# Kernel tuning notes

Hardware: AMD Instinct MI355X
Metric: run time of the kernel (lower is better)

The kernel has to match this reference:

```python
import jax, jax.numpy as jnp
import numpy as np
from jax import lax

ROUTING_ITERS = 3
EPS = 1e-8


def _conv(x, w, b, stride=1):
    # x: [B,C,H,W], w: [O,C,kh,kw]  (VALID padding, NCHW/OIHW)
    y = lax.conv_general_dilated(x, w, (stride, stride), 'VALID',
                                 dimension_numbers=('NCHW', 'OIHW', 'NCHW'))
    return y + b[None, :, None, None]


def _maxpool2(x):
    return lax.reduce_window(x, -jnp.inf, lax.max, (1, 1, 2, 2), (1, 1, 2, 2), 'VALID')


def _squash(s, axis=-1):
    n2 = jnp.sum(s * s, axis=axis, keepdims=True)
    return s * (n2 / (1.0 + n2)) / jnp.sqrt(n2 + EPS)


def setup_inputs() -> dict:
    key = jax.random.key(0)
    ks = jax.random.split(key, 9)
    p = lambda k, shp: (jax.random.normal(k, shp, dtype=jnp.float32) * 0.05)
    return {
        'x':  jax.random.normal(ks[0], (64, 1, 92, 92), dtype=jnp.float32),
        'w1': p(ks[1], (128, 1, 9, 9)),   'b1': jnp.zeros((128,), jnp.float32),
        'w2': p(ks[2], (64, 128, 5, 5)),  'b2': jnp.zeros((64,), jnp.float32),
        'wc': p(ks[3], (128, 64, 8, 8)),  'bc': jnp.zeros((128,), jnp.float32),
        # routing transform: [num_primary=1024, num_sar=10, out_dim=16, in_dim=32]
        'Wr': p(ks[4], (1024, 10, 16, 32)),
    }


def reference(x, w1, b1, w2, b2, wc, bc, Wr):
    B = x.shape[0]
    # feature extractor (dropout is identity at inference)
    h = jax.nn.relu(_conv(x, w1, b1))          # [B,128,84,84]
    h = _maxpool2(h)                            # [B,128,42,42]
    h = _conv(h, w2, b2)                        # [B,64,38,38]
    # primary capsule conv
    h = _conv(h, wc, bc, stride=2)              # [B,128,16,16]
    # 128 channels = 4 capsule types * 32-dim capsules, 16x16 spatial -> 1024 caps
    u = h.reshape(B, 4, 32, 16, 16).transpose(0, 1, 3, 4, 2).reshape(B, 1024, 32)
    u = _squash(u)                              # [B,1024,32]
    # u_hat: predictions of each primary cap for each SAR cap
    u_hat = jnp.einsum('bpi,ptoi->bpto', u, Wr)  # [B,1024,10,16]
    # dynamic routing
    b_log = jnp.zeros((B, 1024, 10), dtype=x.dtype)
    for _ in range(ROUTING_ITERS):
        c = jax.nn.softmax(b_log, axis=2)               # [B,1024,10]
        s = jnp.einsum('bpt,bpto->bto', c, u_hat)       # [B,10,16]
        v = _squash(s)                                   # [B,10,16]
        b_log = b_log + jnp.einsum('bpto,bto->bpt', u_hat, v)
    likelihood = jnp.sqrt(jnp.sum(v * v, axis=-1) + EPS)  # [B,10]
    return likelihood
```

## Files before the change

kernel.cpp:

```cpp
#include <hip/hip_runtime.h>
#include <hip/hip_bf16.h>
#include <math.h>


#define EPSF 1e-8f

typedef __bf16 bf16x8 __attribute__((ext_vector_type(8)));
typedef __bf16 bf16x4 __attribute__((ext_vector_type(4)));
typedef float floatx4 __attribute__((ext_vector_type(4)));
typedef float floatx16 __attribute__((ext_vector_type(16)));

__global__ __launch_bounds__(256) void k_t_all(const float* __restrict__ Wr,
                                               const float* __restrict__ wc,
                                               const float* __restrict__ w2,
                                               const float* __restrict__ w1,
                                               __bf16* __restrict__ wrb,
                                               __bf16* __restrict__ wca,
                                               __bf16* __restrict__ w2a,
                                               __bf16* __restrict__ w1b) {
    int i = blockIdx.x * 256 + threadIdx.x;
    if (i < 5242880) {
        wrb[i] = (__bf16)Wr[i];
        return;
    }
    int i2 = i - 5242880;
    if (i2 < 524288) {
        int j = i2 & 7, lane = (i2 >> 3) & 63, f = i2 >> 9;
        int ct = f & 3, ks = (f >> 2) & 1, khw = (f >> 3) & 63, icc = f >> 9;
        int c32 = lane & 31, h = lane >> 5;
        int oc = ct * 32 + c32;
        int ic = icc * 32 + ks * 16 + h * 8 + j;
        wca[i2] = (__bf16)wc[(oc * 64 + ic) * 64 + khw];
        return;
    }
    int i3 = i2 - 524288;
    if (i3 < 204800) {
        int j = i3 & 7, lane = (i3 >> 3) & 63, f = i3 >> 9;
        int mt = f & 1, ks = (f >> 1) & 3, rem = f >> 3;
        int khw = rem % 25, icc = rem / 25;
        int c32 = lane & 31, h = lane >> 5;
        int oc = mt * 32 + c32;
        int ic = icc * 64 + ks * 16 + h * 8 + j;
        w2a[i3] = (__bf16)w2[(oc * 128 + ic) * 25 + khw];
        return;
    }
    int i4 = i3 - 204800;
    if (i4 < 12288) {
        int kt = i4 >> 10, oc = (i4 >> 3) & 127, j = i4 & 7;
        int k = kt * 8 + j;
        w1b[i4] = (__bf16)(k < 81 ? w1[oc * 81 + k] : 0.f);
    }
}

__global__ __launch_bounds__(256, 3) void k_conv1_mfma(const float* __restrict__ x,
                                                       const __bf16* __restrict__ w1b,
                                                       const float* __restrict__ b1,
                                                       __bf16* __restrict__ h1n) {
    __shared__ float xs[960];
    __shared__ __bf16 Bl[18432];
    int py = blockIdx.x, b = blockIdx.y;
    int t = threadIdx.x;
    int lane = t & 63, w = t >> 6;
    int cc = lane & 15, q = lane >> 4;

    const float* xb = x + (size_t)b * 8464 + 2 * py * 92;
    for (int j = t; j < 920; j += 256) xs[j] = xb[j];

    bf16x8 af2[2][3];
#pragma unroll
    for (int g2 = 0; g2 < 2; ++g2)
#pragma unroll
        for (int ks = 0; ks < 3; ++ks)
            af2[g2][ks] = *(const bf16x8*)(w1b + ((ks * 4 + q) * 128 + g2 * 64 + w * 16 + cc) * 8);

    __syncthreads();

    if (t < 192) {
        int row = t / 96, pos = t - (t / 96) * 96;
        int sbase = row * 92 + pos;
        bool pvalid = pos < 84;
#pragma unroll
        for (int kt = 0; kt < 12; ++kt) {
            bf16x8 pk;
#pragma unroll
            for (int j = 0; j < 8; ++j) {
                int k = kt * 8 + j;
                int kh = k / 9, kw = k - kh * 9;
                float v = (pvalid && k < 81) ? xs[sbase + kh * 92 + kw] : 0.f;
                pk[j] = (__bf16)v;
            }
            *(bf16x8*)(Bl + ((kt * 2 + row) * 96 + pos) * 8) = pk;
        }
    }
    __syncthreads();

    floatx4 acc[2][2][6];
#pragma unroll
    for (int g2 = 0; g2 < 2; ++g2)
#pragma unroll
        for (int rr = 0; rr < 2; ++rr)
#pragma unroll
            for (int n6 = 0; n6 < 6; ++n6)
                acc[g2][rr][n6] = (floatx4){0.f, 0.f, 0.f, 0.f};

    const char* Bb = (const char*)Bl + cc * 16 + q * 3072;
#pragma unroll
    for (int rr = 0; rr < 2; ++rr)
#pragma unroll
        for (int n6 = 0; n6 < 6; ++n6) {
#pragma unroll
            for (int ks = 0; ks < 3; ++ks) {
                bf16x8 bf = *(const bf16x8*)(Bb + ks * 12288 + rr * 1536 + n6 * 256);
                acc[0][rr][n6] = __builtin_amdgcn_mfma_f32_16x16x32_bf16(af2[0][ks], bf, acc[0][rr][n6], 0, 0, 0);
                acc[1][rr][n6] = __builtin_amdgcn_mfma_f32_16x16x32_bf16(af2[1][ks], bf, acc[1][rr][n6], 0, 0, 0);
            }
        }

#pragma unroll
    for (int g2 = 0; g2 < 2; ++g2) {
        int oc0 = g2 * 64 + w * 16 + q * 4;
        float4 bv = *(const float4*)(b1 + oc0);
        size_t obase = (((size_t)b * 42 + py) * 42) * 128 + oc0;
#pragma unroll
        for (int n6 = 0; n6 < 6; ++n6) {
            bf16x4 pk;
#pragma unroll
            for (int r = 0; r < 4; ++r) {
                float vert = fmaxf(acc[g2][0][n6][r], acc[g2][1][n6][r]);
                float hz = fmaxf(vert, __shfl_xor(vert, 1, 64));
                float pooled = fmaxf(hz + ((const float*)&bv)[r], 0.f);
                pk[r] = (__bf16)pooled;
            }
            if ((cc & 1) == 0) {
                int px = n6 * 8 + (cc >> 1);
                if (px < 42)
                    *(bf16x4*)(h1n + obase + (size_t)px * 128) = pk;
            }
        }
    }
}

__global__ __launch_bounds__(256) void k_conv2(const __bf16* __restrict__ h1n,
                                               const __bf16* __restrict__ w2a,
                                               float* __restrict__ p01) {
    __shared__ __bf16 ins[25704];
    int g = blockIdx.x, b = blockIdx.y, icc = blockIdx.z;
    int row0 = g * 5;
    int t = threadIdx.x;
    int lane = t & 63, w = t >> 6;
    int c32 = lane & 31, h = lane >> 5;
    int validp = (g < 7) ? 190 : 114;
    int ic0 = icc * 64;

    int baseN[2], posi[2];
#pragma unroll
    for (int nt = 0; nt < 2; ++nt) {
        int pi = (w * 2 + nt) * 32 + c32;
        int pc = pi < validp ? pi : validp - 1;
        int r = pc / 38, c = pc - r * 38;
        posi[nt] = pi;
        baseN[nt] = (r * 42 + c) * 136 + h * 16;
    }

#pragma unroll
    for (int half = 0; half < 2; ++half) {
        uint4 rb[6];
        int lo[6];
#pragma unroll
        for (int k = 0; k < 6; ++k) {
            int j = (half * 6 + k) * 256 + t;
            if (j > 3023) j -= 256;
            int lr = j / 336, rem = j - lr * 336;
            int ix = rem >> 3, sb = rem & 7;
            int rg = row0 + lr; if (rg > 41) rg = 41;
            rb[k] = *(const uint4*)(h1n + ((((size_t)b * 42 + rg) * 42 + ix) * 128 + ic0 + sb * 8));
            lo[k] = (lr * 42 + ix) * 136 + sb * 16;
        }
#pragma unroll
        for (int k = 0; k < 6; ++k)
            *(uint4*)((char*)ins + lo[k]) = rb[k];
    }

    floatx16 acc[2][2];
#pragma unroll
    for (int mt = 0; mt < 2; ++mt)
#pragma unroll
        for (int nt = 0; nt < 2; ++nt)
#pragma unroll
            for (int i = 0; i < 16; ++i) acc[mt][nt][i] = 0.f;

    const __bf16* wic = w2a + (size_t)icc * 25 * 4096 + (lane << 3);

    bf16x8 abuf[3][8];
#pragma unroll
    for (int ks = 0; ks < 4; ++ks) {
        abuf[0][ks * 2]     = *(const bf16x8*)(wic + 0 * 4096 + ks * 1024);
        abuf[0][ks * 2 + 1] = *(const bf16x8*)(wic + 0 * 4096 + ks * 1024 + 512);
        abuf[1][ks * 2]     = *(const bf16x8*)(wic + 1 * 4096 + ks * 1024);
        abuf[1][ks * 2 + 1] = *(const bf16x8*)(wic + 1 * 4096 + ks * 1024 + 512);
    }

    __syncthreads();
#pragma unroll
    for (int khw = 0; khw < 25; ++khw) {
        if (khw + 2 < 25) {
            const __bf16* wk2 = wic + (khw + 2) * 4096;
#pragma unroll
            for (int ks = 0; ks < 4; ++ks) {
                abuf[(khw + 2) % 3][ks * 2]     = *(const bf16x8*)(wk2 + ks * 1024);
                abuf[(khw + 2) % 3][ks * 2 + 1] = *(const bf16x8*)(wk2 + ks * 1024 + 512);
            }
        }
        int kh = khw / 5, kw = khw - kh * 5;
        int doff = (kh * 42 + kw) * 136;
#pragma unroll
        for (int ks = 0; ks < 4; ++ks) {
            bf16x8 a0 = abuf[khw % 3][ks * 2];
            bf16x8 a1 = abuf[khw % 3][ks * 2 + 1];
#pragma unroll
            for (int nt = 0; nt < 2; ++nt) {
                bf16x8 bfr = *(const bf16x8*)((char*)ins + baseN[nt] + doff + ks * 32);
                acc[0][nt] = __builtin_amdgcn_mfma_f32_32x32x16_bf16(a0, bfr, acc[0][nt], 0, 0, 0);
                acc[1][nt] = __builtin_amdgcn_mfma_f32_32x32x16_bf16(a1, bfr, acc[1][nt], 0, 0, 0);
            }
        }
    }
    float* pdst = p01 + (size_t)icc * 5914624;
#pragma unroll
    for (int nt = 0; nt < 2; ++nt) {
        int pi = posi[nt];
        if (pi < validp) {
            int r = pi / 38, c = pi - r * 38;
            int oh = row0 + r;
            size_t obase = (((size_t)b * 38 + oh) * 38 + c) * 64;
#pragma unroll
            for (int mt = 0; mt < 2; ++mt) {
#pragma unroll
                for (int g2 = 0; g2 < 4; ++g2) {
                    int oc0 = mt * 32 + g2 * 8 + h * 4;
                    floatx4 pv;
                    pv[0] = acc[mt][nt][g2 * 4 + 0];
                    pv[1] = acc[mt][nt][g2 * 4 + 1];
                    pv[2] = acc[mt][nt][g2 * 4 + 2];
                    pv[3] = acc[mt][nt][g2 * 4 + 3];
                    *(floatx4*)(pdst + obase + oc0) = pv;
                }
            }
        }
    }
}

__global__ __launch_bounds__(256) void k_reduce_h2(const float* __restrict__ p01,
                                                   const float* __restrict__ b2,
                                                   __bf16* __restrict__ h2n) {
    int i = blockIdx.x * 256 + threadIdx.x;
    if (i >= 1478656) return;
    size_t e = (size_t)i * 4;
    floatx4 a = *(const floatx4*)(p01 + e);
    floatx4 b = *(const floatx4*)(p01 + 5914624 + e);
    floatx4 bv = *(const floatx4*)(b2 + ((i * 4) & 63));
    bf16x4 pk;
    pk.x = (__bf16)(a[0] + b[0] + bv[0]);
    pk.y = (__bf16)(a[1] + b[1] + bv[1]);
    pk.z = (__bf16)(a[2] + b[2] + bv[2]);
    pk.w = (__bf16)(a[3] + b[3] + bv[3]);
    *(bf16x4*)(h2n + e) = pk;
}

__global__ __launch_bounds__(256, 4) void k_convcaps(const __bf16* __restrict__ h2n,
                                                     const __bf16* __restrict__ wca,
                                                     float* __restrict__ pc) {
    __shared__ __bf16 ins[13680];
    int g = blockIdx.x, b = blockIdx.y, icc = blockIdx.z;
    int t = threadIdx.x;
    int lane = t & 63, ct = t >> 6;
    int c32 = lane & 31, h = lane >> 5;
    int rloc = c32 >> 4, cx = c32 & 15;
    int ic0 = icc * 32;

    floatx16 acc;
#pragma unroll
    for (int i = 0; i < 16; ++i) acc[i] = 0.f;

    int Bbase = (76 * rloc + cx) * 72 + h * 16;
    {
        uint4 rb[6];
        int lo[6];
#pragma unroll
        for (int k = 0; k < 6; ++k) {
            int j = k * 256 + t;
            if (j > 1519) j -= 256;
            int r = j / 152, rem = j - r * 152;
            int c = rem >> 2, s = rem & 3;
            rb[k] = *(const uint4*)(h2n + ((((size_t)b * 38 + 4 * g + r) * 38 + c) * 64 + ic0 + s * 8));
            int X = (r * 2 + (c & 1)) * 19 + (c >> 1);
            lo[k] = X * 72 + s * 16;
        }
#pragma unroll
        for (int k = 0; k < 6; ++k)
            *(uint4*)((char*)ins + lo[k]) = rb[k];
    }
    __syncthreads();
    const __bf16* wic = wca + ((size_t)icc * 64 * 8 + ct) * 512 + (lane << 3);
#pragma unroll
    for (int khw = 0; khw < 64; ++khw) {
        int kh = khw >> 3, kw = khw & 7;
        int par = kw & 1, k2 = kw >> 1;
        int doff = ((kh * 2 + par) * 19 + k2) * 72;
        const __bf16* wk = wic + khw * 4096;
#pragma unroll
        for (int ks = 0; ks < 2; ++ks) {
            bf16x8 af = *(const bf16x8*)(wk + ks * 2048);
            bf16x8 bfr = *(const bf16x8*)((char*)ins + Bbase + doff + ks * 32);
            acc = __builtin_amdgcn_mfma_f32_32x32x16_bf16(af, bfr, acc, 0, 0, 0);
        }
    }
    int pos = (2 * g + rloc) * 16 + cx;
    float* dst = pc + (size_t)icc * 2097152 + (((size_t)b * 1024 + ct * 256 + pos) * 32);
#pragma unroll
    for (int g2 = 0; g2 < 4; ++g2) {
        floatx4 pv;
        pv[0] = acc[g2 * 4 + 0];
        pv[1] = acc[g2 * 4 + 1];
        pv[2] = acc[g2 * 4 + 2];
        pv[3] = acc[g2 * 4 + 3];
        *(floatx4*)(dst + g2 * 8 + h * 4) = pv;
    }
}

__global__ __launch_bounds__(256) void k_squash(const float* __restrict__ pc,
                                                const float* __restrict__ bc,
                                                __bf16* __restrict__ ub) {
    int i = blockIdx.x * 256 + threadIdx.x;
    if (i >= 65536) return;
    int ct = (i >> 8) & 3;
    const float* p0 = pc + (size_t)i * 32;
    const float* p1 = pc + 2097152 + (size_t)i * 32;
    const float* bv = bc + ct * 32;
    float vals[32];
    float n2 = 0.f;
#pragma unroll
    for (int k = 0; k < 8; ++k) {
        floatx4 a = *(const floatx4*)(p0 + k * 4);
        floatx4 b = *(const floatx4*)(p1 + k * 4);
        floatx4 bb = *(const floatx4*)(bv + k * 4);
#pragma unroll
        for (int e = 0; e < 4; ++e) {
            float v = a[e] + b[e] + bb[e];
            vals[k * 4 + e] = v;
            n2 = fmaf(v, v, n2);
        }
    }
    float scale = (n2 / (1.f + n2)) / sqrtf(n2 + EPSF);
    __bf16* dst = ub + (size_t)i * 32;
#pragma unroll
    for (int k = 0; k < 8; ++k) {
        bf16x4 pk;
        pk.x = (__bf16)(vals[k * 4 + 0] * scale);
        pk.y = (__bf16)(vals[k * 4 + 1] * scale);
        pk.z = (__bf16)(vals[k * 4 + 2] * scale);
        pk.w = (__bf16)(vals[k * 4 + 3] * scale);
        *(bf16x4*)(dst + k * 4) = pk;
    }
}

__global__ __launch_bounds__(256, 2) void k_uhat(const __bf16* __restrict__ ub,
                                                 const __bf16* __restrict__ wrb,
                                                 __bf16* __restrict__ uhT) {
    int pt = blockIdx.x, ts = blockIdx.y, bz = blockIdx.z;
    int t = threadIdx.x;
    int p = pt * 64 + (t & 63);
    int q = t >> 6;
    bf16x8 wf[4][4];
#pragma unroll
    for (int o4 = 0; o4 < 4; ++o4)
#pragma unroll
        for (int j = 0; j < 4; ++j)
            wf[o4][j] = *(const bf16x8*)(wrb + (((size_t)p * 10 + ts) * 16 + q * 4 + o4) * 32 + j * 8);
#pragma unroll 1
    for (int bi = 0; bi < 16; ++bi) {
        int b = bz * 16 + bi;
        bf16x8 uf[4];
        const bf16x8* up = (const bf16x8*)(ub + ((size_t)b * 1024 + p) * 32);
#pragma unroll
        for (int j = 0; j < 4; ++j) uf[j] = up[j];
        float sv[4];
#pragma unroll
        for (int o4 = 0; o4 < 4; ++o4) {
            float s = 0.f;
#pragma unroll
            for (int j = 0; j < 4; ++j)
#pragma unroll
                for (int e = 0; e < 8; ++e)
                    s = fmaf((float)uf[j][e], (float)wf[o4][j][e], s);
            sv[o4] = s;
        }
        bf16x4 pk;
        pk.x = (__bf16)sv[0];
        pk.y = (__bf16)sv[1];
        pk.z = (__bf16)sv[2];
        pk.w = (__bf16)sv[3];
        *(bf16x4*)(uhT + ((((size_t)b * 10 + ts) * 1024 + p) * 16 + q * 4)) = pk;
    }
}

#define UHS_ADDR(P, HF) ((((P) << 5) + ((HF) << 4)) ^ ((((P) >> 2) & 7) << 4))
__global__ __launch_bounds__(256) void k_route(const __bf16* __restrict__ uhT,
                                               const float* __restrict__ blR,
                                               float* __restrict__ blW,
                                               float* __restrict__ out,
                                               int first, int dob, int last) {
    __shared__ __bf16 uh_s[16384];
    __shared__ float sred[4][16];
    __shared__ float vs[16];
    int b = blockIdx.x, tt = blockIdx.y;
    int t = threadIdx.x;
    const __bf16* uhb = uhT + ((size_t)b * 10 + tt) * 16384;
#pragma unroll
    for (int k = 0; k < 8; ++k) {
        int j = k * 256 + t;
        *(uint4*)((char*)uh_s + UHS_ADDR(j >> 1, j & 1)) =
            *(const uint4*)((const char*)uhb + j * 16);
    }
    __syncthreads();

    float acc[16];
#pragma unroll
    for (int o = 0; o < 16; ++o) acc[o] = 0.f;
    const float* blb = blR + b * 10240;
    for (int p = t; p < 1024; p += 256) {
        float c;
        if (first) {
            c = 0.1f;
        } else {
            float den = 0.f, et = 0.f;
#pragma unroll
            for (int tp = 0; tp < 10; ++tp) {
                float e = expf(blb[tp * 1024 + p]);
                den += e;
                if (tp == tt) et = e;
            }
            c = et / den;
        }
        bf16x8 u0 = *(const bf16x8*)((char*)uh_s + UHS_ADDR(p, 0));
        bf16x8 u1 = *(const bf16x8*)((char*)uh_s + UHS_ADDR(p, 1));
#pragma unroll
        for (int o = 0; o < 8; ++o) {
            acc[o]     = fmaf(c, (float)u0[o], acc[o]);
            acc[8 + o] = fmaf(c, (float)u1[o], acc[8 + o]);
        }
    }
    int lane = t & 63, wid = t >> 6;
#pragma unroll
    for (int o = 0; o < 16; ++o) {
        float v = acc[o];
#pragma unroll
        for (int off = 32; off >= 1; off >>= 1) v += __shfl_xor(v, off, 64);
        if (lane == 0) sred[wid][o] = v;
    }
    __syncthreads();
    if (t < 16) {
        float s = (sred[0][t] + sred[1][t]) + (sred[2][t] + sred[3][t]);
        float n2 = s * s;
#pragma unroll
        for (int off = 1; off < 16; off <<= 1) n2 += __shfl_xor(n2, off, 16);
        float scale = (n2 / (1.f + n2)) / sqrtf(n2 + EPSF);
        vs[t] = s * scale;
        if (last && t == 0) {
            float sv2 = n2 * scale * scale;
            out[b * 10 + tt] = sqrtf(sv2 + EPSF);
        }
    }
    __syncthreads();

    if (dob) {
        const float* blr = blR + (b * 10 + tt) * 1024;
        float* blw = blW + (b * 10 + tt) * 1024;
        for (int p = t; p < 1024; p += 256) {
            bf16x8 u0 = *(const bf16x8*)((char*)uh_s + UHS_ADDR(p, 0));
            bf16x8 u1 = *(const bf16x8*)((char*)uh_s + UHS_ADDR(p, 1));
            float d = 0.f;
#pragma unroll
            for (int o = 0; o < 8; ++o) {
                d = fmaf((float)u0[o], vs[o], d);
                d = fmaf((float)u1[o], vs[8 + o], d);
            }
            blw[p] = first ? d : (blr[p] + d);
        }
    }
}

extern "C" void kernel_launch(void* const* d_in, const int* in_sizes, int n_in,
                              void* d_out, int out_size, void* d_ws, size_t ws_size,
                              hipStream_t stream) {
    const float* x  = (const float*)d_in[0];
    const float* w1 = (const float*)d_in[1];
    const float* b1 = (const float*)d_in[2];
    const float* w2 = (const float*)d_in[3];
    const float* b2 = (const float*)d_in[4];
    const float* wc = (const float*)d_in[5];
    const float* bc = (const float*)d_in[6];
    const float* Wr = (const float*)d_in[7];
    float* out = (float*)d_out;
    float* ws  = (float*)d_ws;

    __bf16* w2a = (__bf16*)(ws);
    __bf16* wca = (__bf16*)(ws + 102400);
    __bf16* w1b = (__bf16*)(ws + 364544);
    __bf16* h1n = (__bf16*)(ws + 375040);
    __bf16* h2n = (__bf16*)(ws + 7600384);
    __bf16* ub  = (__bf16*)(ws + 12654848);
    float*  blA = ws + 14752000;
    __bf16* wrb = (__bf16*)(ws + 15417600);
    float*  p01 = ws + 18039040;
    float*  pc  = ws + 18039040;
    float*  blB = ws + 29868288;
    __bf16* uhT = (__bf16*)(ws + 375040);

    k_t_all<<<23376, 256, 0, stream>>>(Wr, wc, w2, w1, wrb, wca, w2a, w1b);
    k_conv1_mfma<<<dim3(42, 64), 256, 0, stream>>>(x, w1b, b1, h1n);
    k_conv2<<<dim3(8, 64, 2), 256, 0, stream>>>(h1n, w2a, p01);
    k_reduce_h2<<<5776, 256, 0, stream>>>(p01, b2, h2n);
    k_convcaps<<<dim3(8, 64, 2), 256, 0, stream>>>(h2n, wca, pc);
    k_squash<<<256, 256, 0, stream>>>(pc, bc, ub);
    k_uhat<<<dim3(16, 10, 4), 256, 0, stream>>>(ub, wrb, uhT);
    k_route<<<dim3(64, 10), 256, 0, stream>>>(uhT, blA, blA, out, 1, 1, 0);
    k_route<<<dim3(64, 10), 256, 0, stream>>>(uhT, blA, blB, out, 0, 1, 0);
    k_route<<<dim3(64, 10), 256, 0, stream>>>(uhT, blB, blB, out, 0, 0, 1);
}
```

Measured before the change: 283.0 us.

## Compute u_hat with bf16 MFMA using pre-swizzled routing weights

Replaces the scalar FMA u_hat kernel with one that issues a 16x16x32 bf16 MFMA per (primary capsule, SAR type). The weight-conversion kernel now writes Wr in an MFMA fragment layout so each lane loads one contiguous 8-element vector. Each wave handles 16 batch columns, and the grid becomes 64x10 blocks without a batch split. This trades the register-resident weight reuse across batches for matrix-core throughput and a changed memory access pattern.

```diff
diff --git a/kernel.cpp b/kernel.cpp
--- a/kernel.cpp
+++ b/kernel.cpp
@@ -20,7 +20,10 @@
                                                __bf16* __restrict__ w1b) {
     int i = blockIdx.x * 256 + threadIdx.x;
     if (i < 5242880) {
-        wrb[i] = (__bf16)Wr[i];
+        int e = i & 7, l = (i >> 3) & 63;
+        int pt_ = i >> 9;
+        int o = l & 15, k = (l >> 4) * 8 + e;
+        wrb[i] = (__bf16)Wr[((size_t)pt_ * 16 + o) * 32 + k];
         return;
     }
     int i2 = i - 5242880;
@@ -364,43 +367,29 @@
     }
 }
 
-__global__ __launch_bounds__(256, 2) void k_uhat(const __bf16* __restrict__ ub,
-                                                 const __bf16* __restrict__ wrb,
-                                                 __bf16* __restrict__ uhT) {
-    int pt = blockIdx.x, ts = blockIdx.y, bz = blockIdx.z;
+__global__ __launch_bounds__(256) void k_uhat(const __bf16* __restrict__ ub,
+                                              const __bf16* __restrict__ wrf,
+                                              __bf16* __restrict__ uhT) {
+    int pg = blockIdx.x, ts = blockIdx.y;
     int t = threadIdx.x;
-    int p = pt * 64 + (t & 63);
-    int q = t >> 6;
-    bf16x8 wf[4][4];
-#pragma unroll
-    for (int o4 = 0; o4 < 4; ++o4)
-#pragma unroll
-        for (int j = 0; j < 4; ++j)
-            wf[o4][j] = *(const bf16x8*)(wrb + (((size_t)p * 10 + ts) * 16 + q * 4 + o4) * 32 + j * 8);
-#pragma unroll 1
-    for (int bi = 0; bi < 16; ++bi) {
-        int b = bz * 16 + bi;
-        bf16x8 uf[4];
-        const bf16x8* up = (const bf16x8*)(ub + ((size_t)b * 1024 + p) * 32);
-#pragma unroll
-        for (int j = 0; j < 4; ++j) uf[j] = up[j];
-        float sv[4];
-#pragma unroll
-        for (int o4 = 0; o4 < 4; ++o4) {
-            float s = 0.f;
-#pragma unroll
-            for (int j = 0; j < 4; ++j)
-#pragma unroll
-                for (int e = 0; e < 8; ++e)
-                    s = fmaf((float)uf[j][e], (float)wf[o4][j][e], s);
-            sv[o4] = s;
-        }
+    int lane = t & 63, bt = t >> 6;
+    int bcol = bt * 16 + (lane & 15);
+    int ko = lane >> 4;
+    const __bf16* ubase = ub + (size_t)bcol * 32768 + ko * 8;
+    __bf16* obase = uhT + ((size_t)bcol * 10 + ts) * 16384 + ko * 4;
+#pragma unroll 4
+    for (int i = 0; i < 16; ++i) {
+        int p = pg * 16 + i;
+        bf16x8 a = *(const bf16x8*)(wrf + (((size_t)p * 10 + ts) * 64 + lane) * 8);
+        bf16x8 bb = *(const bf16x8*)(ubase + (size_t)p * 32);
+        floatx4 c = (floatx4){0.f, 0.f, 0.f, 0.f};
+        c = __builtin_amdgcn_mfma_f32_16x16x32_bf16(a, bb, c, 0, 0, 0);
         bf16x4 pk;
-        pk.x = (__bf16)sv[0];
-        pk.y = (__bf16)sv[1];
-        pk.z = (__bf16)sv[2];
-        pk.w = (__bf16)sv[3];
-        *(bf16x4*)(uhT + ((((size_t)b * 10 + ts) * 1024 + p) * 16 + q * 4)) = pk;
+        pk.x = (__bf16)c[0];
+        pk.y = (__bf16)c[1];
+        pk.z = (__bf16)c[2];
+        pk.w = (__bf16)c[3];
+        *(bf16x4*)(obase + (size_t)p * 16) = pk;
     }
 }
 
@@ -523,7 +512,7 @@
     k_reduce_h2<<<5776, 256, 0, stream>>>(p01, b2, h2n);
     k_convcaps<<<dim3(8, 64, 2), 256, 0, stream>>>(h2n, wca, pc);
     k_squash<<<256, 256, 0, stream>>>(pc, bc, ub);
-    k_uhat<<<dim3(16, 10, 4), 256, 0, stream>>>(ub, wrb, uhT);
+    k_uhat<<<dim3(64, 10), 256, 0, stream>>>(ub, wrb, uhT);
     k_route<<<dim3(64, 10), 256, 0, stream>>>(uhT, blA, blA, out, 1, 1, 0);
     k_route<<<dim3(64, 10), 256, 0, stream>>>(uhT, blA, blB, out, 0, 1, 0);
     k_route<<<dim3(64, 10), 256, 0, stream>>>(uhT, blB, blB, out, 0, 0, 1);
```

New measurement: 273.4 us. 1.04x faster.
